# Kernel optimization log

Measured on AMD Instinct MI355X. Metric: run time of the kernel, lower is better.

Reference implementation:

```python
import jax, jax.numpy as jnp
import numpy as np

N = 50000
E = 400000
F_IN = 5
H = 8
C1, C2, C3 = 64, 32, 16
NEG_SLOPE = 0.2


def setup_inputs() -> dict:
    key = jax.random.key(0)
    ks = jax.random.split(key, 16)
    s = 0.1  # small init scale
    return {
        "x": jax.random.normal(ks[0], (N, F_IN), jnp.float32),
        "edge_index": jax.random.randint(ks[1], (2, E), 0, N, jnp.int64),
        "edge_weight": jax.random.uniform(ks[2], (E,), jnp.float32),
        "W1": jax.random.normal(ks[3], (F_IN, H * C1), jnp.float32) * s,
        "a_src1": jax.random.normal(ks[4], (H, C1), jnp.float32) * s,
        "a_dst1": jax.random.normal(ks[5], (H, C1), jnp.float32) * s,
        "b1": jnp.zeros((H * C1,), jnp.float32),
        "W2": jax.random.normal(ks[6], (H * C1, H * C2), jnp.float32) * s,
        "a_src2": jax.random.normal(ks[7], (H, C2), jnp.float32) * s,
        "a_dst2": jax.random.normal(ks[8], (H, C2), jnp.float32) * s,
        "b2": jnp.zeros((H * C2,), jnp.float32),
        "Wg": jax.random.normal(ks[9], (H * C2, C3), jnp.float32) * s,
        "bg": jnp.zeros((C3,), jnp.float32),
        "Wfc": jax.random.normal(ks[10], (C3, 1), jnp.float32) * s,
        "bfc": jnp.zeros((1,), jnp.float32),
    }


def _gat_layer(x, W, a_src, a_dst, b, src, dst, n, heads, ch):
    # PyG GATConv (concat=True), eval mode (dropout off), self-loops already in src/dst.
    h = (x @ W).reshape(n, heads, ch)                      # (N, H, C)
    e_s = jnp.sum(h * a_src, axis=-1)                      # (N, H)
    e_d = jnp.sum(h * a_dst, axis=-1)                      # (N, H)
    e = jax.nn.leaky_relu(e_s[src] + e_d[dst], NEG_SLOPE)  # (Etot, H)
    m = jax.ops.segment_max(e, dst, num_segments=n)
    m = jnp.where(jnp.isfinite(m), m, 0.0)                 # guard empty segments
    ex = jnp.exp(e - m[dst])
    den = jax.ops.segment_sum(ex, dst, num_segments=n)
    alpha = ex / (den[dst] + 1e-16)                        # softmax over in-edges
    out = jax.ops.segment_sum(h[src] * alpha[..., None], dst, num_segments=n)
    return out.reshape(n, heads * ch) + b


def _gcn_layer(x, W, b, src, dst, w_full, n):
    # PyG GCNConv with gcn_norm: D^{-1/2} A_hat D^{-1/2}, self-loop weight 1.
    deg = jax.ops.segment_sum(w_full, dst, num_segments=n)
    dinv = jnp.where(deg > 0, jax.lax.rsqrt(deg), 0.0)
    norm = dinv[src] * w_full * dinv[dst]                  # (Etot,)
    h = x @ W                                              # (N, C3)
    out = jax.ops.segment_sum(h[src] * norm[:, None], dst, num_segments=n)
    return out + b


def reference(x, edge_index, edge_weight, W1, a_src1, a_dst1, b1,
              W2, a_src2, a_dst2, b2, Wg, bg, Wfc, bfc):
    n = x.shape[0]
    loops = jnp.arange(n, dtype=edge_index.dtype)
    src = jnp.concatenate([edge_index[0], loops])
    dst = jnp.concatenate([edge_index[1], loops])
    w_full = jnp.concatenate([edge_weight, jnp.ones((n,), edge_weight.dtype)])

    h = _gat_layer(x, W1, a_src1, a_dst1, b1, src, dst, n, H, C1)
    h = jax.nn.elu(h)
    h = _gat_layer(h, W2, a_src2, a_dst2, b2, src, dst, n, H, C2)
    h = jax.nn.elu(h)
    h = _gcn_layer(h, Wg, bg, src, dst, w_full, n)
    h = jax.nn.elu(h)
    out = jax.nn.sigmoid(h @ Wfc + bfc)                    # (N, 1)
    return out
```

## Files before the change

kernel.cpp:

```cpp
#include <hip/hip_runtime.h>
#include <hip/hip_bf16.h>
#include <float.h>
#include <math.h>

#define N_NODES 50000
#define N_EDGES 400000
#define ETOT    (N_EDGES + N_NODES)
#define F_IN    5
#define HEADS   8
#define C1      64
#define C2      32
#define C3      16
#define HC1     (HEADS * C1)
#define HC2     (HEADS * C2)
#define NEG_SLOPE 0.2f
#define NCHUNK  ((N_NODES + 255) / 256)
#define NH8     (N_NODES * HEADS)
#define MPAD    (((N_NODES + 63) / 64) * 64)
#define GCOLS   (HC2 + 16)
#define PACKBLK ((GCOLS * HC1) / 256)
#define SCATBLK ((ETOT + 255) / 256)
#define ES1BLK  ((NH8 + 255) / 256)
#define INIT_DEG  SCATBLK
#define INIT_W2X  (INIT_DEG + PACKBLK)
#define INIT_TOT  (INIT_W2X + ES1BLK)

#define WFIX_SCALE 68719476736.0f
#define WFIX_MASK  ((1ULL << 46) - 1)

typedef short bf16x8 __attribute__((ext_vector_type(8)));
typedef float f32x4  __attribute__((ext_vector_type(4)));
typedef unsigned short ushort_t;
typedef unsigned short ushort8_t __attribute__((ext_vector_type(8)));

__device__ __forceinline__ float eluf(float x) {
    return x > 0.f ? x : (expf(x) - 1.f);
}
__device__ __forceinline__ float bf2f(unsigned short u) {
    union { unsigned int i; float f; } v; v.i = ((unsigned int)u) << 16; return v.f;
}
__device__ __forceinline__ unsigned short f2bf(float f) {
    __hip_bfloat16 b = __float2bfloat16(f);
    return *(unsigned short*)&b;
}
__device__ __forceinline__ float softnum(float es, float ed) {
    float v = es + ed;
    v = v > 0.f ? v : NEG_SLOPE * v;
    return expf(v);
}

__global__ void k_init(const int* __restrict__ ei, const float* __restrict__ ew,
                       unsigned long long* __restrict__ pack,
                       ushort_t* __restrict__ rank,
                       const float* __restrict__ x, float* __restrict__ xp8,
                       const float* __restrict__ W2,
                       const float* __restrict__ a_src2, const float* __restrict__ a_dst2,
                       ushort_t* __restrict__ W2X,
                       const float* __restrict__ W1,
                       const float* __restrict__ a_src1, const float* __restrict__ a_dst1,
                       float* __restrict__ es, float* __restrict__ ed) {
    __shared__ float asl[HEADS * F_IN], adl[HEADS * F_IN];
    int b = blockIdx.x;
    int t = threadIdx.x;
    if (b < INIT_DEG) {
        int i = b * 256 + t;
        if (i >= ETOT) return;
        int d;
        float w;
        if (i < N_EDGES) { d = ei[N_EDGES + i]; w = ew[i]; }
        else             { d = i - N_EDGES;     w = 1.f; }
        unsigned long long enc =
            (1ULL << 46) | (unsigned long long)(w * WFIX_SCALE + 0.5f);
        unsigned long long old = atomicAdd(&pack[d], enc);
        rank[i] = (ushort_t)(old >> 46);
    } else if (b < INIT_W2X) {
        int idx = (b - INIT_DEG) * 256 + t;
        int c = idx >> 9;
        int k = idx & 511;
        float v;
        if (c < HC2) {
            v = W2[(size_t)k * HC2 + c];
        } else {
            int h = (c - HC2) & 7;
            const float* av = (c < HC2 + 8) ? a_src2 : a_dst2;
            v = 0.f;
#pragma unroll 8
            for (int j = 0; j < C2; j++)
                v += W2[(size_t)k * HC2 + h * C2 + j] * av[h * C2 + j];
        }
        W2X[idx] = f2bf(v);
    } else {
        if (t < HEADS * F_IN) {
            int h = t / F_IN, f = t % F_IN;
            float s = 0.f, dv = 0.f;
            for (int c = 0; c < C1; c++) {
                float wv = W1[f * HC1 + h * C1 + c];
                s  += wv * a_src1[h * C1 + c];
                dv += wv * a_dst1[h * C1 + c];
            }
            asl[t] = s;
            adl[t] = dv;
        }
        __syncthreads();
        int g = (b - INIT_W2X) * 256 + t;
        if (g < NH8) {
            int n = g >> 3, h = g & 7;
            float vs = 0.f, vd = 0.f;
#pragma unroll
            for (int f = 0; f < F_IN; f++) {
                float xv = x[n * F_IN + f];
                vs += xv * asl[h * F_IN + f];
                vd += xv * adl[h * F_IN + f];
            }
            es[g] = vs;
            ed[g] = vd;
            xp8[g] = (h < F_IN) ? x[n * F_IN + h] : 0.f;
        }
    }
}

__global__ void k_scan_a(const unsigned long long* __restrict__ pack,
                         int* __restrict__ part) {
    __shared__ int lds[256];
    int t = threadIdx.x;
    int i = blockIdx.x * 256 + t;
    lds[t] = (i < N_NODES) ? (int)(pack[i] >> 46) : 0;
    __syncthreads();
    for (int off = 128; off >= 1; off >>= 1) {
        if (t < off) lds[t] += lds[t + off];
        __syncthreads();
    }
    if (t == 0) part[blockIdx.x] = lds[0];
}

__global__ void k_scan_b(int* part) {
    __shared__ int lds[256];
    int t = threadIdx.x;
    int v = (t < NCHUNK) ? part[t] : 0;
    lds[t] = v;
    __syncthreads();
    for (int off = 1; off < 256; off <<= 1) {
        int x = (t >= off) ? lds[t - off] : 0;
        __syncthreads();
        lds[t] += x;
        __syncthreads();
    }
    if (t < NCHUNK) part[t] = lds[t] - v;
}

__global__ void k_scan_c(const unsigned long long* __restrict__ pack,
                         const int* __restrict__ part,
                         int* __restrict__ offs, float* __restrict__ dinv) {
    __shared__ int lds[256];
    int t = threadIdx.x;
    int i = blockIdx.x * 256 + t;
    unsigned long long p = (i < N_NODES) ? pack[i] : 0ULL;
    int v = (int)(p >> 46);
    lds[t] = v;
    __syncthreads();
    for (int off = 1; off < 256; off <<= 1) {
        int x = (t >= off) ? lds[t - off] : 0;
        __syncthreads();
        lds[t] += x;
        __syncthreads();
    }
    int excl = part[blockIdx.x] + lds[t] - v;
    if (i < N_NODES) {
        offs[i] = excl;
        float ws = (float)(p & WFIX_MASK) * (1.0f / WFIX_SCALE);
        dinv[i] = ws > 0.f ? rsqrtf(ws) : 0.f;
    }
    if (i == N_NODES - 1) offs[N_NODES] = excl + v;
}

__global__ void k_scatter(const int* __restrict__ ei, const int* __restrict__ offs,
                          const ushort_t* __restrict__ rank, int2* __restrict__ csr,
                          const float* __restrict__ ew, const float* __restrict__ dinv) {
    int i = blockIdx.x * 256 + threadIdx.x;
    if (i >= ETOT) return;
    int s, d;
    float w;
    if (i < N_EDGES) { s = ei[i]; d = ei[N_EDGES + i]; w = ew[i]; }
    else             { s = d = i - N_EDGES; w = 1.f; }
    float nrm = dinv[s] * w * dinv[d];
    int pos = offs[d] + (int)rank[i];
    csr[pos] = make_int2(s, __float_as_int(nrm));
}

__global__ __launch_bounds__(256) void k_aggexp(const float* __restrict__ xp8,
                                                const float* __restrict__ es1,
                                                const float* __restrict__ ed1,
                                                const int* __restrict__ offs,
                                                const int2* __restrict__ csr,
                                                const float* __restrict__ W1,
                                                const float* __restrict__ b1,
                                                ushort_t* __restrict__ x2bf) {
    __shared__ float ax[256 * F_IN];
    int t = threadIdx.x;
    int g = blockIdx.x * 256 + t;
    if (g < NH8) {
        int d = g >> 3, h = g & 7;
        float edv = ed1[g];
        int k0 = offs[d], k1 = offs[d + 1];
        float a0 = 0.f, a1 = 0.f, a2 = 0.f, a3 = 0.f, a4 = 0.f, exsum = 0.f;
        int k = k0;
        if (k + 1 < k1) {
            int2 c0 = csr[k], c1 = csr[k + 1];
            for (; k + 3 < k1; k += 2) {
                int2 n0 = csr[k + 2], n1 = csr[k + 3];
                float x0 = softnum(es1[c0.x * HEADS + h], edv);
                float x1 = softnum(es1[c1.x * HEADS + h], edv);
                float4 A0 = *(const float4*)(xp8 + (size_t)c0.x * 8);
                float  B0 = xp8[(size_t)c0.x * 8 + 4];
                float4 A1 = *(const float4*)(xp8 + (size_t)c1.x * 8);
                float  B1 = xp8[(size_t)c1.x * 8 + 4];
                a0 += x0 * A0.x + x1 * A1.x;
                a1 += x0 * A0.y + x1 * A1.y;
                a2 += x0 * A0.z + x1 * A1.z;
                a3 += x0 * A0.w + x1 * A1.w;
                a4 += x0 * B0   + x1 * B1;
                exsum += x0 + x1;
                c0 = n0; c1 = n1;
            }
            {
                float x0 = softnum(es1[c0.x * HEADS + h], edv);
                float x1 = softnum(es1[c1.x * HEADS + h], edv);
                float4 A0 = *(const float4*)(xp8 + (size_t)c0.x * 8);
                float  B0 = xp8[(size_t)c0.x * 8 + 4];
                float4 A1 = *(const float4*)(xp8 + (size_t)c1.x * 8);
                float  B1 = xp8[(size_t)c1.x * 8 + 4];
                a0 += x0 * A0.x + x1 * A1.x;
                a1 += x0 * A0.y + x1 * A1.y;
                a2 += x0 * A0.z + x1 * A1.z;
                a3 += x0 * A0.w + x1 * A1.w;
                a4 += x0 * B0   + x1 * B1;
                exsum += x0 + x1;
                k += 2;
            }
        }
        if (k < k1) {
            int2 c0 = csr[k];
            float x0 = softnum(es1[c0.x * HEADS + h], edv);
            float4 A0 = *(const float4*)(xp8 + (size_t)c0.x * 8);
            float  B0 = xp8[(size_t)c0.x * 8 + 4];
            a0 += x0 * A0.x;
            a1 += x0 * A0.y;
            a2 += x0 * A0.z;
            a3 += x0 * A0.w;
            a4 += x0 * B0;
            exsum += x0;
        }
        float inv = 1.f / (exsum + 1e-16f);
        float* ap = ax + t * F_IN;
        ap[0] = a0 * inv;
        ap[1] = a1 * inv;
        ap[2] = a2 * inv;
        ap[3] = a3 * inv;
        ap[4] = a4 * inv;
    }
    __syncthreads();
    int wave = t >> 6, j = t & 63;
    int n0 = blockIdx.x * 32;
    int h = j >> 3;
    const float* w1p = W1 + j * 8;
#pragma unroll 1
    for (int it = 0; it < 8; ++it) {
        int nl = wave * 8 + it;
        int n = n0 + nl;
        if (n >= N_NODES) break;
        const float* ap = ax + (nl * 8 + h) * F_IN;
        float av[F_IN];
#pragma unroll
        for (int f = 0; f < F_IN; f++) av[f] = ap[f];
        float4 s0 = *(const float4*)(b1 + j * 8);
        float4 s1 = *(const float4*)(b1 + j * 8 + 4);
#pragma unroll
        for (int f = 0; f < F_IN; f++) {
            float4 w0  = *(const float4*)(w1p + f * HC1);
            float4 w1v = *(const float4*)(w1p + f * HC1 + 4);
            s0.x += av[f] * w0.x;  s0.y += av[f] * w0.y;
            s0.z += av[f] * w0.z;  s0.w += av[f] * w0.w;
            s1.x += av[f] * w1v.x; s1.y += av[f] * w1v.y;
            s1.z += av[f] * w1v.z; s1.w += av[f] * w1v.w;
        }
        ushort8_t o;
        o[0] = f2bf(eluf(s0.x)); o[1] = f2bf(eluf(s0.y));
        o[2] = f2bf(eluf(s0.z)); o[3] = f2bf(eluf(s0.w));
        o[4] = f2bf(eluf(s1.x)); o[5] = f2bf(eluf(s1.y));
        o[6] = f2bf(eluf(s1.z)); o[7] = f2bf(eluf(s1.w));
        *(ushort8_t*)(x2bf + (size_t)n * HC1 + j * 8) = o;
    }
}

__global__ __launch_bounds__(256, 3) void k_gemm_mfma(const short* __restrict__ A,
                                                      const short* __restrict__ W2X,
                                                      ushort_t* __restrict__ h2bf,
                                                      float* __restrict__ es2,
                                                      float* __restrict__ ed2) {
    __shared__ short Bs[GCOLS * 32];
    int t    = threadIdx.x;
    int wave = t >> 6;
    int lane = t & 63;
    int lo   = lane & 15;
    int quad = lane >> 4;
    int m0   = blockIdx.x * 64 + wave * 16;
    const short* ap = A + (size_t)(m0 + lo) * HC1 + quad * 8;

    f32x4 acc[17];
#pragma unroll
    for (int f = 0; f < 17; f++) acc[f] = (f32x4){0.f, 0.f, 0.f, 0.f};

    for (int idx = t; idx < GCOLS * 4; idx += 256) {
        int c = idx >> 2, q = idx & 3;
        int s = (q + c + (c >> 2)) & 3;
        *(bf16x8*)(Bs + c * 32 + s * 8) = *(const bf16x8*)(W2X + (size_t)c * HC1 + q * 8);
    }
    __syncthreads();

#pragma unroll 1
    for (int k0 = 0; k0 < HC1; k0 += 32) {
        int nk = k0 + 32;
        bf16x8 pre[5];
        if (nk < HC1) {
#pragma unroll
            for (int j = 0; j < 5; j++) {
                int idx = t + j * 256;
                if (idx < GCOLS * 4) {
                    int c = idx >> 2, q = idx & 3;
                    pre[j] = *(const bf16x8*)(W2X + (size_t)c * HC1 + nk + q * 8);
                }
            }
        }
        bf16x8 aF = *(const bf16x8*)(ap + k0);
#pragma unroll
        for (int f = 0; f < 17; f++) {
            int c = f * 16 + lo;
            int s = (quad + c + (c >> 2)) & 3;
            bf16x8 bF = *(const bf16x8*)(Bs + c * 32 + s * 8);
            acc[f] = __builtin_amdgcn_mfma_f32_16x16x32_bf16(aF, bF, acc[f], 0, 0, 0);
        }
        __syncthreads();
        if (nk < HC1) {
#pragma unroll
            for (int j = 0; j < 5; j++) {
                int idx = t + j * 256;
                if (idx < GCOLS * 4) {
                    int c = idx >> 2, q = idx & 3;
                    int s = (q + c + (c >> 2)) & 3;
                    *(bf16x8*)(Bs + c * 32 + s * 8) = pre[j];
                }
            }
            __syncthreads();
        }
    }

    int rowb = m0 + quad * 4;
#pragma unroll
    for (int f = 0; f < 16; f++) {
#pragma unroll
        for (int r = 0; r < 4; r++) {
            int row = rowb + r;
            if (row < N_NODES)
                h2bf[(size_t)row * HC2 + f * 16 + lo] = f2bf(acc[f][r]);
        }
    }
#pragma unroll
    for (int r = 0; r < 4; r++) {
        int row = rowb + r;
        if (row < N_NODES) {
            if (lo < 8) es2[row * HEADS + lo]       = acc[16][r];
            else        ed2[row * HEADS + (lo - 8)] = acc[16][r];
        }
    }
}

__global__ __launch_bounds__(128) void k_gat_agg2(const ushort_t* __restrict__ h2bf,
                                                  const float* __restrict__ es2,
                                                  const float* __restrict__ ed2,
                                                  const int* __restrict__ offs,
                                                  const int2* __restrict__ csr,
                                                  const float* __restrict__ b2,
                                                  ushort_t* __restrict__ x3bf) {
    int wave = threadIdx.x >> 6;
    int lane = threadIdx.x & 63;
    int d = blockIdx.x * 2 + wave;
    if (d >= N_NODES) return;
    int c4 = lane * 4;
    int h  = lane >> 3;
    float edv = ed2[d * HEADS + h];
    int k0 = offs[d], k1 = offs[d + 1];
    float acc0 = 0.f, acc1 = 0.f, acc2 = 0.f, acc3 = 0.f, exsum = 0.f;
    int k = k0;
    for (; k + 3 < k1; k += 4) {
        int2 e0 = csr[k], e1 = csr[k + 1], e2 = csr[k + 2], e3 = csr[k + 3];
        float r0 = es2[e0.x * HEADS + h];
        float r1 = es2[e1.x * HEADS + h];
        float r2 = es2[e2.x * HEADS + h];
        float r3 = es2[e3.x * HEADS + h];
        ushort4 v0 = *(const ushort4*)(h2bf + (size_t)e0.x * HC2 + c4);
        ushort4 v1 = *(const ushort4*)(h2bf + (size_t)e1.x * HC2 + c4);
        ushort4 v2 = *(const ushort4*)(h2bf + (size_t)e2.x * HC2 + c4);
        ushort4 v3 = *(const ushort4*)(h2bf + (size_t)e3.x * HC2 + c4);
        float x0 = softnum(r0, edv);
        float x1 = softnum(r1, edv);
        float x2 = softnum(r2, edv);
        float x3 = softnum(r3, edv);
        acc0 += x0 * bf2f(v0.x) + x1 * bf2f(v1.x) + x2 * bf2f(v2.x) + x3 * bf2f(v3.x);
        acc1 += x0 * bf2f(v0.y) + x1 * bf2f(v1.y) + x2 * bf2f(v2.y) + x3 * bf2f(v3.y);
        acc2 += x0 * bf2f(v0.z) + x1 * bf2f(v1.z) + x2 * bf2f(v2.z) + x3 * bf2f(v3.z);
        acc3 += x0 * bf2f(v0.w) + x1 * bf2f(v1.w) + x2 * bf2f(v2.w) + x3 * bf2f(v3.w);
        exsum += (x0 + x1) + (x2 + x3);
    }
    for (; k < k1; k++) {
        int2 e0 = csr[k];
        float x0 = softnum(es2[e0.x * HEADS + h], edv);
        ushort4 v0 = *(const ushort4*)(h2bf + (size_t)e0.x * HC2 + c4);
        acc0 += x0 * bf2f(v0.x);
        acc1 += x0 * bf2f(v0.y);
        acc2 += x0 * bf2f(v0.z);
        acc3 += x0 * bf2f(v0.w);
        exsum += x0;
    }
    float inv = 1.f / (exsum + 1e-16f);
    float4 bias = *(const float4*)(b2 + c4);
    ushort4 o;
    o.x = f2bf(eluf(acc0 * inv + bias.x));
    o.y = f2bf(eluf(acc1 * inv + bias.y));
    o.z = f2bf(eluf(acc2 * inv + bias.z));
    o.w = f2bf(eluf(acc3 * inv + bias.w));
    *(ushort4*)(x3bf + (size_t)d * HC2 + c4) = o;
}

__global__ __launch_bounds__(256) void k_hg(const ushort_t* __restrict__ x3bf,
                                            const float* __restrict__ Wg,
                                            float* __restrict__ hg) {
    __shared__ float xs[16 * 260];
    int n0 = blockIdx.x * 16;
    int t  = threadIdx.x;
    for (int q = t; q < 16 * HC2 / 4; q += 256) {
        int r  = q >> 6;
        int cc = (q & 63) * 4;
        int n  = n0 + r;
        ushort4 v = make_ushort4(0, 0, 0, 0);
        if (n < N_NODES) v = *(const ushort4*)(x3bf + (size_t)n * HC2 + cc);
        xs[r * 260 + cc + 0] = bf2f(v.x);
        xs[r * 260 + cc + 1] = bf2f(v.y);
        xs[r * 260 + cc + 2] = bf2f(v.z);
        xs[r * 260 + cc + 3] = bf2f(v.w);
    }
    __syncthreads();
    int r = t >> 4, c = t & 15;
    const float* xr = xs + r * 260;
    float acc = 0.f;
#pragma unroll 8
    for (int k = 0; k < HC2; k += 4) {
        float4 v = *(const float4*)(xr + k);
        acc += v.x * Wg[(k + 0) * C3 + c];
        acc += v.y * Wg[(k + 1) * C3 + c];
        acc += v.z * Wg[(k + 2) * C3 + c];
        acc += v.w * Wg[(k + 3) * C3 + c];
    }
    int n = n0 + r;
    if (n < N_NODES) hg[(size_t)n * C3 + c] = acc;
}

__global__ __launch_bounds__(256) void k_gcn_out(const float* __restrict__ hg,
                                                 const int* __restrict__ offs,
                                                 const int2* __restrict__ csr,
                                                 const float* __restrict__ bg,
                                                 const float* __restrict__ Wfc,
                                                 const float* __restrict__ bfc,
                                                 float* __restrict__ out) {
    int t = threadIdx.x;
    int r = t >> 4, c = t & 15;
    int d = blockIdx.x * 16 + r;
    float val = 0.f;
    if (d < N_NODES) {
        int k0 = offs[d], k1 = offs[d + 1];
        float acc = 0.f;
        int k = k0;
        if (k + 1 < k1) {
            int2 e0 = csr[k], e1 = csr[k + 1];
            for (; k + 3 < k1; k += 2) {
                int2 n0 = csr[k + 2], n1 = csr[k + 3];
                acc += hg[(size_t)e0.x * C3 + c] * __int_as_float(e0.y);
                acc += hg[(size_t)e1.x * C3 + c] * __int_as_float(e1.y);
                e0 = n0; e1 = n1;
            }
            acc += hg[(size_t)e0.x * C3 + c] * __int_as_float(e0.y);
            acc += hg[(size_t)e1.x * C3 + c] * __int_as_float(e1.y);
            k += 2;
        }
        if (k < k1) {
            int2 e0 = csr[k];
            acc += hg[(size_t)e0.x * C3 + c] * __int_as_float(e0.y);
        }
        val = eluf(acc + bg[c]);
    }
    float z = val * Wfc[c];
#pragma unroll
    for (int off = 8; off >= 1; off >>= 1) z += __shfl_xor(z, off, 16);
    if (c == 0 && d < N_NODES) out[d] = 1.f / (1.f + expf(-(z + bfc[0])));
}

extern "C" void kernel_launch(void* const* d_in, const int* in_sizes, int n_in,
                              void* d_out, int out_size, void* d_ws, size_t ws_size,
                              hipStream_t stream) {
    const float* x       = (const float*)d_in[0];
    const int*   ei      = (const int*)  d_in[1];
    const float* ew      = (const float*)d_in[2];
    const float* W1      = (const float*)d_in[3];
    const float* a_src1  = (const float*)d_in[4];
    const float* a_dst1  = (const float*)d_in[5];
    const float* b1      = (const float*)d_in[6];
    const float* W2      = (const float*)d_in[7];
    const float* a_src2  = (const float*)d_in[8];
    const float* a_dst2  = (const float*)d_in[9];
    const float* b2      = (const float*)d_in[10];
    const float* Wg      = (const float*)d_in[11];
    const float* bg      = (const float*)d_in[12];
    const float* Wfc     = (const float*)d_in[13];
    const float* bfc     = (const float*)d_in[14];
    float* out = (float*)d_out;

    char* w = (char*)d_ws;
    size_t off = 0;
    auto alloc = [&](size_t bytes) -> void* {
        void* p = w + off;
        off = (off + bytes + 255) & ~(size_t)255;
        return p;
    };
    ushort_t* x2bf = (ushort_t*)alloc((size_t)MPAD * HC1 * 2);
    ushort_t* W2X  = (ushort_t*)alloc((size_t)GCOLS * HC1 * 2);
    ushort_t* h2bf = (ushort_t*)alloc((size_t)N_NODES * HC2 * 2);
    ushort_t* x3bf = (ushort_t*)alloc((size_t)N_NODES * HC2 * 2);
    float* hg     = (float*)alloc((size_t)N_NODES * C3 * 4);
    float* es1    = (float*)alloc((size_t)NH8 * 4);
    float* ed1    = (float*)alloc((size_t)NH8 * 4);
    float* es2    = (float*)alloc((size_t)NH8 * 4);
    float* ed2    = (float*)alloc((size_t)NH8 * 4);
    unsigned long long* pack = (unsigned long long*)alloc((size_t)N_NODES * 8);
    char*  zero_end = w + off;
    ushort_t* rank = (ushort_t*)alloc((size_t)ETOT * 2);
    int*   offs   = (int*)  alloc((size_t)(N_NODES + 1) * 4);
    int*   part   = (int*)  alloc(256 * 4);
    int2*  csr    = (int2*) alloc((size_t)ETOT * 8);
    float* dinv   = (float*)alloc((size_t)N_NODES * 4);
    float* xp8    = (float*)alloc((size_t)N_NODES * 8 * 4);

    hipMemsetAsync(pack, 0, (size_t)(zero_end - (char*)pack), stream);
    k_init<<<dim3(INIT_TOT), dim3(256), 0, stream>>>(
        ei, ew, pack, rank, x, xp8, W2, a_src2, a_dst2, W2X,
        W1, a_src1, a_dst1, es1, ed1);
    k_scan_a<<<dim3(NCHUNK), dim3(256), 0, stream>>>(pack, part);
    k_scan_b<<<dim3(1), dim3(256), 0, stream>>>(part);
    k_scan_c<<<dim3(NCHUNK), dim3(256), 0, stream>>>(pack, part, offs, dinv);
    k_scatter<<<dim3(SCATBLK), dim3(256), 0, stream>>>(ei, offs, rank, csr, ew, dinv);

    k_aggexp<<<dim3(ES1BLK), dim3(256), 0, stream>>>(
        xp8, es1, ed1, offs, csr, W1, b1, x2bf);

    k_gemm_mfma<<<dim3(MPAD / 64), dim3(256), 0, stream>>>(
        (const short*)x2bf, (const short*)W2X, h2bf, es2, ed2);
    k_gat_agg2<<<dim3((N_NODES + 1) / 2), dim3(128), 0, stream>>>(
        h2bf, es2, ed2, offs, csr, b2, x3bf);

    k_hg<<<dim3((N_NODES + 15) / 16), dim3(256), 0, stream>>>(x3bf, Wg, hg);
    k_gcn_out<<<dim3((N_NODES + 15) / 16), dim3(256), 0, stream>>>(
        hg, offs, csr, bg, Wfc, bfc, out);
}
```

Measured before the change: 279.3 us.

## Merge three-pass scan into one block and drop self-loop atomics

Replaces the three-kernel degree scan with a single 1024-thread block in which each thread serially handles 49 nodes. Self-loops no longer go through atomics: each node adds one to its count and weight, and its self-loop is placed in the last CSR slot of its row. The aggregation loops in the first GAT layer and the GCN output are also restructured to load four edges per iteration instead of using two-deep software prefetch. This removes two kernel launches and 50k atomics, but the single-block scan runs serially on one CU with strided, uncoalesced loads.

```diff
diff --git a/kernel.cpp b/kernel.cpp
--- a/kernel.cpp
+++ b/kernel.cpp
@@ -14,19 +14,21 @@
 #define HC1     (HEADS * C1)
 #define HC2     (HEADS * C2)
 #define NEG_SLOPE 0.2f
-#define NCHUNK  ((N_NODES + 255) / 256)
 #define NH8     (N_NODES * HEADS)
 #define MPAD    (((N_NODES + 63) / 64) * 64)
 #define GCOLS   (HC2 + 16)
 #define PACKBLK ((GCOLS * HC1) / 256)
 #define SCATBLK ((ETOT + 255) / 256)
 #define ES1BLK  ((NH8 + 255) / 256)
-#define INIT_DEG  SCATBLK
+#define INIT_DEG  ((N_EDGES + 255) / 256)
 #define INIT_W2X  (INIT_DEG + PACKBLK)
 #define INIT_TOT  (INIT_W2X + ES1BLK)
 
 #define WFIX_SCALE 68719476736.0f
 #define WFIX_MASK  ((1ULL << 46) - 1)
+
+#define SCAN_T   1024
+#define SCAN_PER 49
 
 typedef short bf16x8 __attribute__((ext_vector_type(8)));
 typedef float f32x4  __attribute__((ext_vector_type(4)));
@@ -64,11 +66,9 @@
     int t = threadIdx.x;
     if (b < INIT_DEG) {
         int i = b * 256 + t;
-        if (i >= ETOT) return;
-        int d;
-        float w;
-        if (i < N_EDGES) { d = ei[N_EDGES + i]; w = ew[i]; }
-        else             { d = i - N_EDGES;     w = 1.f; }
+        if (i >= N_EDGES) return;
+        int d   = ei[N_EDGES + i];
+        float w = ew[i];
         unsigned long long enc =
             (1ULL << 46) | (unsigned long long)(w * WFIX_SCALE + 0.5f);
         unsigned long long old = atomicAdd(&pack[d], enc);
@@ -119,58 +119,37 @@
     }
 }
 
-__global__ void k_scan_a(const unsigned long long* __restrict__ pack,
-                         int* __restrict__ part) {
-    __shared__ int lds[256];
-    int t = threadIdx.x;
-    int i = blockIdx.x * 256 + t;
-    lds[t] = (i < N_NODES) ? (int)(pack[i] >> 46) : 0;
+__global__ __launch_bounds__(1024) void k_scan(const unsigned long long* __restrict__ pack,
+                                               int* __restrict__ offs,
+                                               float* __restrict__ dinv) {
+    __shared__ int ws[SCAN_T];
+    int t  = threadIdx.x;
+    int i0 = t * SCAN_PER;
+    int lsum = 0;
+    for (int j = 0; j < SCAN_PER; j++) {
+        int i = i0 + j;
+        if (i < N_NODES) lsum += (int)(pack[i] >> 46) + 1;
+    }
+    ws[t] = lsum;
     __syncthreads();
-    for (int off = 128; off >= 1; off >>= 1) {
-        if (t < off) lds[t] += lds[t + off];
+    for (int off = 1; off < SCAN_T; off <<= 1) {
+        int v = (t >= off) ? ws[t - off] : 0;
         __syncthreads();
-    }
-    if (t == 0) part[blockIdx.x] = lds[0];
-}
-
-__global__ void k_scan_b(int* part) {
-    __shared__ int lds[256];
-    int t = threadIdx.x;
-    int v = (t < NCHUNK) ? part[t] : 0;
-    lds[t] = v;
-    __syncthreads();
-    for (int off = 1; off < 256; off <<= 1) {
-        int x = (t >= off) ? lds[t - off] : 0;
+        ws[t] += v;
         __syncthreads();
-        lds[t] += x;
-        __syncthreads();
-    }
-    if (t < NCHUNK) part[t] = lds[t] - v;
-}
-
-__global__ void k_scan_c(const unsigned long long* __restrict__ pack,
-                         const int* __restrict__ part,
-                         int* __restrict__ offs, float* __restrict__ dinv) {
-    __shared__ int lds[256];
-    int t = threadIdx.x;
-    int i = blockIdx.x * 256 + t;
-    unsigned long long p = (i < N_NODES) ? pack[i] : 0ULL;
-    int v = (int)(p >> 46);
-    lds[t] = v;
-    __syncthreads();
-    for (int off = 1; off < 256; off <<= 1) {
-        int x = (t >= off) ? lds[t - off] : 0;
-        __syncthreads();
-        lds[t] += x;
-        __syncthreads();
-    }
-    int excl = part[blockIdx.x] + lds[t] - v;
-    if (i < N_NODES) {
-        offs[i] = excl;
-        float ws = (float)(p & WFIX_MASK) * (1.0f / WFIX_SCALE);
-        dinv[i] = ws > 0.f ? rsqrtf(ws) : 0.f;
-    }
-    if (i == N_NODES - 1) offs[N_NODES] = excl + v;
+    }
+    int run = ws[t] - lsum;
+    for (int j = 0; j < SCAN_PER; j++) {
+        int i = i0 + j;
+        if (i < N_NODES) {
+            unsigned long long p = pack[i];
+            offs[i] = run;
+            run += (int)(p >> 46) + 1;
+            float wsum = (float)(p & WFIX_MASK) * (1.0f / WFIX_SCALE) + 1.0f;
+            dinv[i] = rsqrtf(wsum);
+        }
+    }
+    if (i0 < N_NODES && i0 + SCAN_PER >= N_NODES) offs[N_NODES] = run;
 }
 
 __global__ void k_scatter(const int* __restrict__ ei, const int* __restrict__ offs,
@@ -178,12 +157,16 @@
                           const float* __restrict__ ew, const float* __restrict__ dinv) {
     int i = blockIdx.x * 256 + threadIdx.x;
     if (i >= ETOT) return;
-    int s, d;
+    int s, d, pos;
     float w;
-    if (i < N_EDGES) { s = ei[i]; d = ei[N_EDGES + i]; w = ew[i]; }
-    else             { s = d = i - N_EDGES; w = 1.f; }
+    if (i < N_EDGES) {
+        s = ei[i]; d = ei[N_EDGES + i]; w = ew[i];
+        pos = offs[d] + (int)rank[i];
+    } else {
+        s = d = i - N_EDGES; w = 1.f;
+        pos = offs[d + 1] - 1;
+    }
     float nrm = dinv[s] * w * dinv[d];
-    int pos = offs[d] + (int)rank[i];
     csr[pos] = make_int2(s, __float_as_int(nrm));
 }
 
@@ -204,41 +187,32 @@
         int k0 = offs[d], k1 = offs[d + 1];
         float a0 = 0.f, a1 = 0.f, a2 = 0.f, a3 = 0.f, a4 = 0.f, exsum = 0.f;
         int k = k0;
-        if (k + 1 < k1) {
-            int2 c0 = csr[k], c1 = csr[k + 1];
-            for (; k + 3 < k1; k += 2) {
-                int2 n0 = csr[k + 2], n1 = csr[k + 3];
-                float x0 = softnum(es1[c0.x * HEADS + h], edv);
-                float x1 = softnum(es1[c1.x * HEADS + h], edv);
-                float4 A0 = *(const float4*)(xp8 + (size_t)c0.x * 8);
-                float  B0 = xp8[(size_t)c0.x * 8 + 4];
-                float4 A1 = *(const float4*)(xp8 + (size_t)c1.x * 8);
-                float  B1 = xp8[(size_t)c1.x * 8 + 4];
-                a0 += x0 * A0.x + x1 * A1.x;
-                a1 += x0 * A0.y + x1 * A1.y;
-                a2 += x0 * A0.z + x1 * A1.z;
-                a3 += x0 * A0.w + x1 * A1.w;
-                a4 += x0 * B0   + x1 * B1;
-                exsum += x0 + x1;
-                c0 = n0; c1 = n1;
-            }
-            {
-                float x0 = softnum(es1[c0.x * HEADS + h], edv);
-                float x1 = softnum(es1[c1.x * HEADS + h], edv);
-                float4 A0 = *(const float4*)(xp8 + (size_t)c0.x * 8);
-                float  B0 = xp8[(size_t)c0.x * 8 + 4];
-                float4 A1 = *(const float4*)(xp8 + (size_t)c1.x * 8);
-                float  B1 = xp8[(size_t)c1.x * 8 + 4];
-                a0 += x0 * A0.x + x1 * A1.x;
-                a1 += x0 * A0.y + x1 * A1.y;
-                a2 += x0 * A0.z + x1 * A1.z;
-                a3 += x0 * A0.w + x1 * A1.w;
-                a4 += x0 * B0   + x1 * B1;
-                exsum += x0 + x1;
-                k += 2;
-            }
-        }
-        if (k < k1) {
+        for (; k + 3 < k1; k += 4) {
+            int2 c0 = csr[k], c1 = csr[k + 1], c2 = csr[k + 2], c3 = csr[k + 3];
+            float r0 = es1[c0.x * HEADS + h];
+            float r1 = es1[c1.x * HEADS + h];
+            float r2 = es1[c2.x * HEADS + h];
+            float r3 = es1[c3.x * HEADS + h];
+            float4 A0 = *(const float4*)(xp8 + (size_t)c0.x * 8);
+            float  B0 = xp8[(size_t)c0.x * 8 + 4];
+            float4 A1 = *(const float4*)(xp8 + (size_t)c1.x * 8);
+            float  B1 = xp8[(size_t)c1.x * 8 + 4];
+            float4 A2 = *(const float4*)(xp8 + (size_t)c2.x * 8);
+            float  B2 = xp8[(size_t)c2.x * 8 + 4];
+            float4 A3 = *(const float4*)(xp8 + (size_t)c3.x * 8);
+            float  B3 = xp8[(size_t)c3.x * 8 + 4];
+            float x0 = softnum(r0, edv);
+            float x1 = softnum(r1, edv);
+            float x2 = softnum(r2, edv);
+            float x3 = softnum(r3, edv);
+            a0 += x0 * A0.x + x1 * A1.x + x2 * A2.x + x3 * A3.x;
+            a1 += x0 * A0.y + x1 * A1.y + x2 * A2.y + x3 * A3.y;
+            a2 += x0 * A0.z + x1 * A1.z + x2 * A2.z + x3 * A3.z;
+            a3 += x0 * A0.w + x1 * A1.w + x2 * A2.w + x3 * A3.w;
+            a4 += x0 * B0   + x1 * B1   + x2 * B2   + x3 * B3;
+            exsum += (x0 + x1) + (x2 + x3);
+        }
+        for (; k < k1; k++) {
             int2 c0 = csr[k];
             float x0 = softnum(es1[c0.x * HEADS + h], edv);
             float4 A0 = *(const float4*)(xp8 + (size_t)c0.x * 8);
@@ -479,19 +453,16 @@
         int k0 = offs[d], k1 = offs[d + 1];
         float acc = 0.f;
         int k = k0;
-        if (k + 1 < k1) {
-            int2 e0 = csr[k], e1 = csr[k + 1];
-            for (; k + 3 < k1; k += 2) {
-                int2 n0 = csr[k + 2], n1 = csr[k + 3];
-                acc += hg[(size_t)e0.x * C3 + c] * __int_as_float(e0.y);
-                acc += hg[(size_t)e1.x * C3 + c] * __int_as_float(e1.y);
-                e0 = n0; e1 = n1;
-            }
-            acc += hg[(size_t)e0.x * C3 + c] * __int_as_float(e0.y);
-            acc += hg[(size_t)e1.x * C3 + c] * __int_as_float(e1.y);
-            k += 2;
-        }
-        if (k < k1) {
+        for (; k + 3 < k1; k += 4) {
+            int2 e0 = csr[k], e1 = csr[k + 1], e2 = csr[k + 2], e3 = csr[k + 3];
+            float g0 = hg[(size_t)e0.x * C3 + c];
+            float g1 = hg[(size_t)e1.x * C3 + c];
+            float g2 = hg[(size_t)e2.x * C3 + c];
+            float g3 = hg[(size_t)e3.x * C3 + c];
+            acc += g0 * __int_as_float(e0.y) + g1 * __int_as_float(e1.y)
+                 + g2 * __int_as_float(e2.y) + g3 * __int_as_float(e3.y);
+        }
+        for (; k < k1; k++) {
             int2 e0 = csr[k];
             acc += hg[(size_t)e0.x * C3 + c] * __int_as_float(e0.y);
         }
@@ -541,9 +512,8 @@
     float* ed2    = (float*)alloc((size_t)NH8 * 4);
     unsigned long long* pack = (unsigned long long*)alloc((size_t)N_NODES * 8);
     char*  zero_end = w + off;
-    ushort_t* rank = (ushort_t*)alloc((size_t)ETOT * 2);
+    ushort_t* rank = (ushort_t*)alloc((size_t)N_EDGES * 2);
     int*   offs   = (int*)  alloc((size_t)(N_NODES + 1) * 4);
-    int*   part   = (int*)  alloc(256 * 4);
     int2*  csr    = (int2*) alloc((size_t)ETOT * 8);
     float* dinv   = (float*)alloc((size_t)N_NODES * 4);
     float* xp8    = (float*)alloc((size_t)N_NODES * 8 * 4);
@@ -552,9 +522,7 @@
     k_init<<<dim3(INIT_TOT), dim3(256), 0, stream>>>(
         ei, ew, pack, rank, x, xp8, W2, a_src2, a_dst2, W2X,
         W1, a_src1, a_dst1, es1, ed1);
-    k_scan_a<<<dim3(NCHUNK), dim3(256), 0, stream>>>(pack, part);
-    k_scan_b<<<dim3(1), dim3(256), 0, stream>>>(part);
-    k_scan_c<<<dim3(NCHUNK), dim3(256), 0, stream>>>(pack, part, offs, dinv);
+    k_scan<<<dim3(1), dim3(SCAN_T), 0, stream>>>(pack, offs, dinv);
     k_scatter<<<dim3(SCATBLK), dim3(256), 0, stream>>>(ei, offs, rank, csr, ew, dinv);
 
     k_aggexp<<<dim3(ES1BLK), dim3(256), 0, stream>>>(
```

Result: slower. 405.0 us (+45.0%).
